# Kernel tuning notes

Hardware: AMD Instinct MI355X
Metric: run time of the kernel (lower is better)

Reference implementation:

```python
import jax, jax.numpy as jnp
import numpy as np

N_NODES = 50000
N_EDGES = 800000
C = 128
NEG_SLOPE = 0.01  # nn.LeakyReLU default


def _init_linear(key, fan_in, fan_out):
    kw, kb = jax.random.split(key)
    lim = 1.0 / np.sqrt(fan_in)
    W = jax.random.uniform(kw, (fan_in, fan_out), jnp.float32, -lim, lim)
    b = jax.random.uniform(kb, (fan_out,), jnp.float32, -lim, lim)
    return W, b


def setup_inputs() -> dict:
    key = jax.random.key(0)
    ks = jax.random.split(key, 10)
    x = jax.random.normal(ks[0], (N_NODES, C), jnp.float32)
    pos = jax.random.normal(ks[1], (N_NODES, 3), jnp.float32)
    edge_index = jax.random.randint(ks[2], (2, N_EDGES), 0, N_NODES, jnp.int64)
    # mlp_h: Linear(C,C) -> LeakyReLU -> Linear(C,3) -> Tanh
    Wh1, bh1 = _init_linear(ks[3], C, C)
    Wh2, bh2 = _init_linear(ks[4], C, 3)
    # mlp_f: Linear(C+3, C) -> LeakyReLU
    Wf, bf = _init_linear(ks[5], C + 3, C)
    # mlp_g: Linear(C,C) -> LeakyReLU -> Linear(C,C)
    Wg1, bg1 = _init_linear(ks[6], C, C)
    Wg2, bg2 = _init_linear(ks[7], C, C)
    return {"x": x, "pos": pos, "edge_index": edge_index,
            "Wh1": Wh1, "bh1": bh1, "Wh2": Wh2, "bh2": bh2,
            "Wf": Wf, "bf": bf,
            "Wg1": Wg1, "bg1": bg1, "Wg2": Wg2, "bg2": bg2}


def reference(x, pos, edge_index, Wh1, bh1, Wh2, bh2, Wf, bf, Wg1, bg1, Wg2, bg2):
    lrelu = lambda t: jax.nn.leaky_relu(t, NEG_SLOPE)
    # delta_i = tanh(mlp_h(x_i))  -> [N, 3]
    delta = jnp.tanh(lrelu(x @ Wh1 + bh1) @ Wh2 + bh2)
    src, dst = edge_index[0], edge_index[1]  # message j -> i (PyG convention)
    # per-edge relative position: pos_j - pos_i + delta_i  -> [E, 3]
    rel = pos[src] - pos[dst] + delta[dst]
    # per-edge message: mlp_f([rel, x_j])  -> [E, C]
    e = lrelu(jnp.concatenate([rel, x[src]], axis=-1) @ Wf + bf)
    # scatter-max aggregate over incoming edges per target node
    agg = jax.ops.segment_max(e, dst, num_segments=N_NODES)
    agg = jnp.where(jnp.isfinite(agg), agg, 0.0)  # empty segments -> 0
    # out_i = mlp_g(agg_i) + x_i
    out = lrelu(agg @ Wg1 + bg1) @ Wg2 + bg2 + x
    return out
```

## Files before the change

### kernel.cpp

```cpp
#include <hip/hip_runtime.h>
#include <cfloat>
#include <cmath>

#define NEG_SLOPE 0.01f

typedef __attribute__((ext_vector_type(8))) short short8;
typedef __attribute__((ext_vector_type(4))) float f32x4;

__device__ __forceinline__ float lrelu(float v) { return v >= 0.0f ? v : NEG_SLOPE * v; }

__device__ __forceinline__ ushort f2b(float f) {
    unsigned u = __float_as_uint(f);
    u += 0x7fffu + ((u >> 16) & 1u);
    return (ushort)(u >> 16);
}
__device__ __forceinline__ float b2f(ushort s) { return __uint_as_float(((unsigned)s) << 16); }

__device__ __forceinline__ void split8(const float* v, short8& hi, short8& lo) {
#pragma unroll
    for (int j = 0; j < 8; ++j) {
        ushort h = f2b(v[j]);
        hi[j] = (short)h;
        lo[j] = (short)f2b(v[j] - b2f(h));
    }
}

__global__ __launch_bounds__(256) void count_wprep_kernel(
    const int* __restrict__ ei,
    const float* __restrict__ Wh1, const float* __restrict__ Wf,
    const float* __restrict__ Wg1, const float* __restrict__ Wg2,
    ushort* __restrict__ WT, int* __restrict__ G, int E, int NBK)
{
    __shared__ int cnt[256];
    const int t = threadIdx.x;
    const int b = blockIdx.x;

    {
        int tt = b * 256 + t;
        int mat = tt >> 14;
        int idx = tt & 16383;
        int n = idx >> 7, k = idx & 127;
        float v;
        if (mat == 0)      v = Wh1[k * 128 + n];
        else if (mat == 1) v = Wf[(k + 3) * 128 + n];
        else if (mat == 2) v = Wg1[k * 128 + n];
        else               v = Wg2[k * 128 + n];
        WT[(tt - idx) + n * 128 + k] = f2b(v);
    }

    cnt[t] = 0;
    __syncthreads();
    for (int e = b * 256 + t; e < E; e += 65536)
        atomicAdd(&cnt[ei[E + e] >> 8], 1);
    __syncthreads();
    if (t < NBK) G[t * 256 + b] = cnt[t];
}

__global__ __launch_bounds__(256) void scanA_kernel(
    const int* __restrict__ G, int* __restrict__ partial)
{
    __shared__ int s[256];
    int i = blockIdx.x * 256 + threadIdx.x;
    s[threadIdx.x] = G[i];
    __syncthreads();
    for (int d = 128; d > 0; d >>= 1) {
        if (threadIdx.x < d) s[threadIdx.x] += s[threadIdx.x + d];
        __syncthreads();
    }
    if (threadIdx.x == 0) partial[blockIdx.x] = s[0];
}

__global__ __launch_bounds__(256) void scanBC_kernel(
    int* __restrict__ G, const int* __restrict__ partial, int NB)
{
    __shared__ int s[256];
    __shared__ int base;
    const int t = threadIdx.x;
    int v = (t < NB) ? partial[t] : 0;
    s[t] = v;
    __syncthreads();
    for (int d = 1; d < 256; d <<= 1) {
        int a = (t >= d) ? s[t - d] : 0;
        __syncthreads();
        s[t] += a;
        __syncthreads();
    }
    if (t == blockIdx.x) base = s[t] - v;
    __syncthreads();

    int i = blockIdx.x * 256 + t;
    int g = G[i];
    s[t] = g;
    __syncthreads();
    for (int d = 1; d < 256; d <<= 1) {
        int a = (t >= d) ? s[t - d] : 0;
        __syncthreads();
        s[t] += a;
        __syncthreads();
    }
    G[i] = base + s[t] - g;
}

__global__ __launch_bounds__(256) void partition_kernel(
    const int* __restrict__ ei, const int* __restrict__ G,
    uint* __restrict__ bpairs, int E, int NBK)
{
    __shared__ int cur[256];
    const int tid = threadIdx.x;
    if (tid < NBK) cur[tid] = G[tid * 256 + blockIdx.x];
    __syncthreads();
    for (int e = blockIdx.x * 256 + tid; e < E; e += 65536) {
        int src = ei[e];
        int dst = ei[E + e];
        int p = atomicAdd(&cur[dst >> 8], 1);
        bpairs[p] = (uint)src | ((uint)(dst & 255) << 24);
    }
}

__global__ __launch_bounds__(256) void bucket_csr_kernel(
    const uint* __restrict__ bpairs, const int* __restrict__ G,
    int* __restrict__ offs, int* __restrict__ srcs, int E, int M, int NBK)
{
    __shared__ int deg[256], scn[256], cur[256];
    const int b = blockIdx.x;
    const int t = threadIdx.x;
    const int base = G[b * 256];
    const int end  = (b + 1 < NBK) ? G[(b + 1) * 256] : E;
    deg[t] = 0;
    __syncthreads();
    for (int p = base + t; p < end; p += 256)
        atomicAdd(&deg[bpairs[p] >> 24], 1);
    __syncthreads();
    scn[t] = deg[t];
    __syncthreads();
    for (int d = 1; d < 256; d <<= 1) {
        int a = (t >= d) ? scn[t - d] : 0;
        __syncthreads();
        scn[t] += a;
        __syncthreads();
    }
    int excl = scn[t] - deg[t];
    cur[t] = excl;
    int node = b * 256 + t;
    if (node < M) offs[node] = base + excl;
    if (node == M - 1 || (b == NBK - 1 && t == 255)) offs[M] = E;
    __syncthreads();
    for (int p = base + t; p < end; p += 256) {
        uint pk = bpairs[p];
        int qpos = atomicAdd(&cur[pk >> 24], 1);
        srcs[base + qpos] = (int)(pk & 0xFFFFFFu);
    }
}


#define GEMM_CORE_REG(ACC, AH, AL)                                              \
    {                                                                           \
        _Pragma("unroll")                                                       \
        for (int ks = 0; ks < 4; ++ks) {                                        \
            _Pragma("unroll")                                                   \
            for (int nt = 0; nt < 8; ++nt) {                                    \
                short8 bfr = *(const short8*)&Bs[(nt * 16 + ln) * 136 + ks * 32 + qd * 8]; \
                ACC[nt] = __builtin_amdgcn_mfma_f32_16x16x32_bf16(AL[ks], bfr, ACC[nt], 0, 0, 0); \
                ACC[nt] = __builtin_amdgcn_mfma_f32_16x16x32_bf16(AH[ks], bfr, ACC[nt], 0, 0, 0); \
            }                                                                   \
        }                                                                       \
    }

#define STAGE_B(WTP)                                                            \
    {                                                                           \
        _Pragma("unroll")                                                       \
        for (int i = 0; i < 8; ++i) {                                           \
            int c = tid + 256 * i;                                              \
            int r = c >> 4, col8 = (c & 15) * 8;                                \
            *(uint4*)&Bs[r * 136 + col8] = *(const uint4*)((WTP) + r * 128 + col8); \
        }                                                                       \
    }

__global__ __launch_bounds__(256) void hy_kernel(
    const float* __restrict__ x, const ushort* __restrict__ Wh1T,
    const float* __restrict__ bh1, const float* __restrict__ Wh2,
    const float* __restrict__ bh2, const ushort* __restrict__ WfxT,
    const float* __restrict__ Wf, const float* __restrict__ pos,
    float* __restrict__ q, ushort* __restrict__ yb, int M)
{
    __shared__ ushort Bs[128 * 136];
    __shared__ ushort yS[64 * 128];
    const int tid = threadIdx.x;
    const int w = tid >> 6, L = tid & 63, qd = L >> 4, ln = L & 15;
    const int row0 = blockIdx.x * 64;
    const int arow = row0 + w * 16 + ln;

    short8 ah[4], al[4];
    {
        const float* base = x + (size_t)((arow < M) ? arow : 0) * 128 + qd * 8;
        float vb[8];
#pragma unroll
        for (int ks = 0; ks < 4; ++ks) {
            float4 v0 = make_float4(0.f, 0.f, 0.f, 0.f), v1 = v0;
            if (arow < M) {
                v0 = *(const float4*)(base + ks * 32);
                v1 = *(const float4*)(base + ks * 32 + 4);
            }
            vb[0] = v0.x; vb[1] = v0.y; vb[2] = v0.z; vb[3] = v0.w;
            vb[4] = v1.x; vb[5] = v1.y; vb[6] = v1.z; vb[7] = v1.w;
            split8(vb, ah[ks], al[ks]);
        }
    }

    STAGE_B(Wh1T);
    __syncthreads();
    f32x4 acc1[8];
#pragma unroll
    for (int nt = 0; nt < 8; ++nt) acc1[nt] = (f32x4){0.f, 0.f, 0.f, 0.f};
    GEMM_CORE_REG(acc1, ah, al);
    __syncthreads();

    STAGE_B(WfxT);
    __syncthreads();
    f32x4 acc2[8];
#pragma unroll
    for (int nt = 0; nt < 8; ++nt) acc2[nt] = (f32x4){0.f, 0.f, 0.f, 0.f};
    GEMM_CORE_REG(acc2, ah, al);
    __syncthreads();

    float* h1s = (float*)Bs;
#pragma unroll
    for (int nt = 0; nt < 8; ++nt) {
        int n = nt * 16 + ln;
        float bias = bh1[n];
#pragma unroll
        for (int r = 0; r < 4; ++r)
            h1s[(w * 16 + qd * 4 + r) * 132 + n] = lrelu(acc1[nt][r] + bias);
    }
#pragma unroll
    for (int r = 0; r < 4; ++r) {
        int m = w * 16 + qd * 4 + r;
        int gm = row0 + m;
        float p0 = 0.f, p1 = 0.f, p2 = 0.f;
        if (gm < M) { p0 = pos[gm * 3]; p1 = pos[gm * 3 + 1]; p2 = pos[gm * 3 + 2]; }
#pragma unroll
        for (int nt = 0; nt < 8; ++nt) {
            int n = nt * 16 + ln;
            yS[m * 128 + n] = f2b(acc2[nt][r] + p0 * Wf[n] + p1 * Wf[128 + n] + p2 * Wf[256 + n]);
        }
    }
    __syncthreads();

    int row = tid & 63, cc = tid >> 6;
    if (cc < 3 && row0 + row < M) {
        float s = 0.f;
#pragma unroll
        for (int k4 = 0; k4 < 32; ++k4) {
            float4 h = *(const float4*)&h1s[row * 132 + k4 * 4];
            s += h.x * Wh2[(k4 * 4 + 0) * 3 + cc] + h.y * Wh2[(k4 * 4 + 1) * 3 + cc]
               + h.z * Wh2[(k4 * 4 + 2) * 3 + cc] + h.w * Wh2[(k4 * 4 + 3) * 3 + cc];
        }
        q[(row0 + row) * 3 + cc] = tanhf(s + bh2[cc]) - pos[(row0 + row) * 3 + cc];
    }
#pragma unroll
    for (int i = 0; i < 4; ++i) {
        int c = tid + 256 * i;
        int r = c >> 4, col8 = (c & 15) * 8;
        if (row0 + r < M)
            *(uint4*)(yb + (size_t)(row0 + r) * 128 + col8) = *(const uint4*)&yS[r * 128 + col8];
    }
}

__global__ __launch_bounds__(256) void midout_kernel(
    const ushort* __restrict__ aggb, const float* __restrict__ qv,
    const float* __restrict__ Wf, const float* __restrict__ bfv,
    const ushort* __restrict__ Wg1T, const float* __restrict__ bg1,
    const ushort* __restrict__ Wg2T, const float* __restrict__ bg2,
    const float* __restrict__ x, float* __restrict__ out, int M)
{
    __shared__ ushort Bs[128 * 136];
    __shared__ ushort Ms[64 * 136];
    const int tid = threadIdx.x;
    const int w = tid >> 6, L = tid & 63, qd = L >> 4, ln = L & 15;
    const int row0 = blockIdx.x * 64;
    const int arow = row0 + w * 16 + ln;

    short8 ah[4], al[4];
    {
        bool ok = arow < M;
        const ushort* base = aggb + (size_t)(ok ? arow : 0) * 128 + qd * 8;
        float q0 = 0.f, q1 = 0.f, q2 = 0.f;
        if (ok) { q0 = qv[arow * 3]; q1 = qv[arow * 3 + 1]; q2 = qv[arow * 3 + 2]; }
        float vb[8];
#pragma unroll
        for (int ks = 0; ks < 4; ++ks) {
            union { uint4 u; ushort s[8]; } a;
            a.u = ok ? *(const uint4*)(base + ks * 32) : make_uint4(0xFF80FF80u, 0xFF80FF80u, 0xFF80FF80u, 0xFF80FF80u);
#pragma unroll
            for (int j = 0; j < 8; ++j) {
                int k = ks * 32 + qd * 8 + j;
                float dec = 0.f;
                if (a.s[j] != 0xFF80u)
                    dec = lrelu(b2f(a.s[j]) + q0 * Wf[k] + q1 * Wf[128 + k] + q2 * Wf[256 + k] + bfv[k]);
                vb[j] = dec;
            }
            split8(vb, ah[ks], al[ks]);
        }
    }

    STAGE_B(Wg1T);
    __syncthreads();
    f32x4 macc[8];
#pragma unroll
    for (int nt = 0; nt < 8; ++nt) macc[nt] = (f32x4){0.f, 0.f, 0.f, 0.f};
    GEMM_CORE_REG(macc, ah, al);
    __syncthreads();

#pragma unroll
    for (int nt = 0; nt < 8; ++nt) {
        int n = nt * 16 + ln;
        float bias = bg1[n];
#pragma unroll
        for (int r = 0; r < 4; ++r)
            Ms[(w * 16 + qd * 4 + r) * 136 + n] = f2b(lrelu(macc[nt][r] + bias));
    }
    STAGE_B(Wg2T);
    __syncthreads();

    short8 a2[4];
#pragma unroll
    for (int ks = 0; ks < 4; ++ks)
        a2[ks] = *(const short8*)&Ms[(w * 16 + ln) * 136 + ks * 32 + qd * 8];

    f32x4 acc2[8];
#pragma unroll
    for (int nt = 0; nt < 8; ++nt) acc2[nt] = (f32x4){0.f, 0.f, 0.f, 0.f};
#pragma unroll
    for (int ks = 0; ks < 4; ++ks) {
#pragma unroll
        for (int nt = 0; nt < 8; ++nt) {
            short8 bfr = *(const short8*)&Bs[(nt * 16 + ln) * 136 + ks * 32 + qd * 8];
            acc2[nt] = __builtin_amdgcn_mfma_f32_16x16x32_bf16(a2[ks], bfr, acc2[nt], 0, 0, 0);
        }
    }
    __syncthreads();

    float* outS = (float*)Bs;
#pragma unroll
    for (int r = 0; r < 4; ++r) {
        int m = w * 16 + qd * 4 + r;
#pragma unroll
        for (int nt = 0; nt < 8; ++nt)
            outS[m * 132 + nt * 16 + ln] = acc2[nt][r];
    }
    __syncthreads();
#pragma unroll
    for (int i = 0; i < 8; ++i) {
        int c = tid + 256 * i;
        int r = c >> 5, col4 = (c & 31) * 4;
        int gr = row0 + r;
        if (gr < M) {
            float4 o = *(const float4*)&outS[r * 132 + col4];
            float4 bv = *(const float4*)(bg2 + col4);
            float4 xv = *(const float4*)(x + (size_t)gr * 128 + col4);
            o.x += bv.x + xv.x; o.y += bv.y + xv.y;
            o.z += bv.z + xv.z; o.w += bv.w + xv.w;
            *(float4*)(out + (size_t)gr * 128 + col4) = o;
        }
    }
}

__global__ __launch_bounds__(256) void agg_kernel(
    const int* __restrict__ offs, const int* __restrict__ srcs,
    const ushort* __restrict__ yb, ushort* __restrict__ aggb, int M)
{
    int wave = threadIdx.x >> 6;
    int lane = threadIdx.x & 63;
    int node = blockIdx.x * 4 + wave;
    if (node >= M) return;
    int o0 = offs[node], o1 = offs[node + 1];
    float a0 = -INFINITY, a1 = -INFINITY;
    const uint* yp = (const uint*)yb;
    int j = o0;
    for (; j + 3 < o1; j += 4) {
        int s0 = srcs[j], s1 = srcs[j + 1], s2 = srcs[j + 2], s3 = srcs[j + 3];
        uint u0 = yp[(size_t)s0 * 64 + lane];
        uint u1 = yp[(size_t)s1 * 64 + lane];
        uint u2 = yp[(size_t)s2 * 64 + lane];
        uint u3 = yp[(size_t)s3 * 64 + lane];
        a0 = fmaxf(a0, fmaxf(fmaxf(__uint_as_float(u0 << 16), __uint_as_float(u1 << 16)),
                             fmaxf(__uint_as_float(u2 << 16), __uint_as_float(u3 << 16))));
        a1 = fmaxf(a1, fmaxf(fmaxf(__uint_as_float(u0 & 0xFFFF0000u), __uint_as_float(u1 & 0xFFFF0000u)),
                             fmaxf(__uint_as_float(u2 & 0xFFFF0000u), __uint_as_float(u3 & 0xFFFF0000u))));
    }
    for (; j < o1; ++j) {
        uint u = yp[(size_t)srcs[j] * 64 + lane];
        a0 = fmaxf(a0, __uint_as_float(u << 16));
        a1 = fmaxf(a1, __uint_as_float(u & 0xFFFF0000u));
    }
    uint pk = (__float_as_uint(a0) >> 16) | (__float_as_uint(a1) & 0xFFFF0000u);
    ((uint*)aggb)[(size_t)node * 64 + lane] = pk;
}

extern "C" void kernel_launch(void* const* d_in, const int* in_sizes, int n_in,
                              void* d_out, int out_size, void* d_ws, size_t ws_size,
                              hipStream_t stream)
{
    const float* x   = (const float*)d_in[0];
    const float* pos = (const float*)d_in[1];
    const int*   ei  = (const int*)d_in[2];
    const float* Wh1 = (const float*)d_in[3];
    const float* bh1 = (const float*)d_in[4];
    const float* Wh2 = (const float*)d_in[5];
    const float* bh2 = (const float*)d_in[6];
    const float* Wf  = (const float*)d_in[7];
    const float* bf  = (const float*)d_in[8];
    const float* Wg1 = (const float*)d_in[9];
    const float* bg1 = (const float*)d_in[10];
    const float* Wg2 = (const float*)d_in[11];
    const float* bg2 = (const float*)d_in[12];
    float* out = (float*)d_out;

    const int M = in_sizes[0] / 128;
    const int E = in_sizes[2] / 2;
    const int NBK = (M + 255) >> 8;

    char* ws = (char*)d_ws;
    size_t off = 0;
    auto alloc = [&](size_t bytes) { void* p = ws + off; off += (bytes + 255) & ~255ull; return p; };
    ushort* yb     = (ushort*)alloc((size_t)M * 128 * sizeof(ushort));
    ushort* aggb   = (ushort*)alloc((size_t)M * 128 * sizeof(ushort));
    ushort* WT     = (ushort*)alloc(4 * 16384 * sizeof(ushort));
    float*  q      = (float*)alloc((size_t)M * 3 * sizeof(float));
    int*    offs   = (int*)alloc((size_t)(M + 1) * sizeof(int));
    int*    G      = (int*)alloc((size_t)NBK * 256 * sizeof(int));
    int*    part   = (int*)alloc(256 * sizeof(int));
    uint*   bpairs = (uint*)alloc((size_t)E * sizeof(uint));
    int*    srcs   = (int*)alloc((size_t)E * sizeof(int));

    const int gb = (M + 63) / 64;

    count_wprep_kernel<<<256, 256, 0, stream>>>(ei, Wh1, Wf, Wg1, Wg2, WT, G, E, NBK);
    scanA_kernel<<<NBK, 256, 0, stream>>>(G, part);
    scanBC_kernel<<<NBK, 256, 0, stream>>>(G, part, NBK);
    partition_kernel<<<256, 256, 0, stream>>>(ei, G, bpairs, E, NBK);
    bucket_csr_kernel<<<NBK, 256, 0, stream>>>(bpairs, G, offs, srcs, E, M, NBK);

    hy_kernel<<<gb, 256, 0, stream>>>(x, WT, bh1, Wh2, bh2,
                                      WT + 16384, Wf, pos, q, yb, M);
    agg_kernel<<<(M + 3) / 4, 256, 0, stream>>>(offs, srcs, yb, aggb, M);
    midout_kernel<<<gb, 256, 0, stream>>>(aggb, q, Wf, bf,
                                          WT + 2 * 16384, bg1,
                                          WT + 3 * 16384, bg2, x, out, M);
}
```

Baseline: 219.1 us.

## Fuse scatter-max aggregation into MLP-g kernel using LDS atomicMax tiles

After: 343.5 us. 56.8% more time.

```diff
diff --git a/kernel.cpp b/kernel.cpp
--- a/kernel.cpp
+++ b/kernel.cpp
@@ -3,6 +3,7 @@
 #include <cmath>
 
 #define NEG_SLOPE 0.01f
+#define C_ELIST 2048
 
 typedef __attribute__((ext_vector_type(8))) short short8;
 typedef __attribute__((ext_vector_type(4))) float f32x4;
@@ -15,6 +16,14 @@
     return (ushort)(u >> 16);
 }
 __device__ __forceinline__ float b2f(ushort s) { return __uint_as_float(((unsigned)s) << 16); }
+
+__device__ __forceinline__ uint encb(uint b) {
+    return (b & 0x80000000u) ? ~b : (b | 0x80000000u);
+}
+__device__ __forceinline__ float decb(uint v) {
+    uint b = (v & 0x80000000u) ? (v ^ 0x80000000u) : ~v;
+    return __uint_as_float(b);
+}
 
 __device__ __forceinline__ void split8(const float* v, short8& hi, short8& lo) {
 #pragma unroll
@@ -117,41 +126,6 @@
     }
 }
 
-__global__ __launch_bounds__(256) void bucket_csr_kernel(
-    const uint* __restrict__ bpairs, const int* __restrict__ G,
-    int* __restrict__ offs, int* __restrict__ srcs, int E, int M, int NBK)
-{
-    __shared__ int deg[256], scn[256], cur[256];
-    const int b = blockIdx.x;
-    const int t = threadIdx.x;
-    const int base = G[b * 256];
-    const int end  = (b + 1 < NBK) ? G[(b + 1) * 256] : E;
-    deg[t] = 0;
-    __syncthreads();
-    for (int p = base + t; p < end; p += 256)
-        atomicAdd(&deg[bpairs[p] >> 24], 1);
-    __syncthreads();
-    scn[t] = deg[t];
-    __syncthreads();
-    for (int d = 1; d < 256; d <<= 1) {
-        int a = (t >= d) ? scn[t - d] : 0;
-        __syncthreads();
-        scn[t] += a;
-        __syncthreads();
-    }
-    int excl = scn[t] - deg[t];
-    cur[t] = excl;
-    int node = b * 256 + t;
-    if (node < M) offs[node] = base + excl;
-    if (node == M - 1 || (b == NBK - 1 && t == 255)) offs[M] = E;
-    __syncthreads();
-    for (int p = base + t; p < end; p += 256) {
-        uint pk = bpairs[p];
-        int qpos = atomicAdd(&cur[pk >> 24], 1);
-        srcs[base + qpos] = (int)(pk & 0xFFFFFFu);
-    }
-}
-
 
 #define GEMM_CORE_REG(ACC, AH, AL)                                              \
     {                                                                           \
@@ -266,42 +240,117 @@
     }
 }
 
-__global__ __launch_bounds__(256) void midout_kernel(
-    const ushort* __restrict__ aggb, const float* __restrict__ qv,
+__global__ __launch_bounds__(256) void midagg_kernel(
+    const uint* __restrict__ bpairs, const int* __restrict__ G,
+    const ushort* __restrict__ yb, const float* __restrict__ qv,
     const float* __restrict__ Wf, const float* __restrict__ bfv,
     const ushort* __restrict__ Wg1T, const float* __restrict__ bg1,
     const ushort* __restrict__ Wg2T, const float* __restrict__ bg2,
-    const float* __restrict__ x, float* __restrict__ out, int M)
+    const float* __restrict__ x, float* __restrict__ out,
+    int M, int E, int NBK)
 {
     __shared__ ushort Bs[128 * 136];
     __shared__ ushort Ms[64 * 136];
+    __shared__ int ecnt;
+    uint* tile  = (uint*)Bs;
+    uint* elist = (uint*)Ms;
     const int tid = threadIdx.x;
     const int w = tid >> 6, L = tid & 63, qd = L >> 4, ln = L & 15;
     const int row0 = blockIdx.x * 64;
-    const int arow = row0 + w * 16 + ln;
+    const int B = row0 >> 8;
+    const int lo = row0 & 255;
+    const uint* yp = (const uint*)yb;
+
+    for (int i = tid; i < 64 * 132; i += 256) tile[i] = 0u;
+    if (tid == 0) ecnt = 0;
+    __syncthreads();
+
+    const int base = G[B * 256];
+    const int end  = (B + 1 < NBK) ? G[(B + 1) * 256] : E;
+
+    for (int p = base + tid; p < end; p += 256) {
+        uint pk = bpairs[p];
+        int dl = (int)(pk >> 24) - lo;
+        if ((unsigned)dl < 64u) {
+            int idx = atomicAdd(&ecnt, 1);
+            if (idx < C_ELIST) elist[idx] = ((uint)dl << 24) | (pk & 0xFFFFFFu);
+        }
+    }
+    __syncthreads();
+    int n = ecnt;
+
+    if (n <= C_ELIST) {
+        for (int i0 = w * 8; i0 < n; i0 += 32) {
+            uint pk[8], u[8];
+#pragma unroll
+            for (int j = 0; j < 8; ++j)
+                pk[j] = (i0 + j < n) ? elist[i0 + j] : 0xFF000000u;
+#pragma unroll
+            for (int j = 0; j < 8; ++j)
+                if ((pk[j] >> 24) < 64u)
+                    u[j] = yp[(size_t)(pk[j] & 0xFFFFFFu) * 64 + L];
+#pragma unroll
+            for (int j = 0; j < 8; ++j) {
+                uint dl = pk[j] >> 24;
+                if (dl < 64u) {
+                    atomicMax(&tile[dl * 132 + 2 * L],     encb(u[j] << 16));
+                    atomicMax(&tile[dl * 132 + 2 * L + 1], encb(u[j] & 0xFFFF0000u));
+                }
+            }
+        }
+    } else {
+        for (int p0 = base + w * 8; p0 < end; p0 += 32) {
+            uint pk[8], u[8];
+#pragma unroll
+            for (int j = 0; j < 8; ++j) {
+                int p = p0 + j;
+                uint raw = (p < end) ? bpairs[p] : 0xFF000000u;
+                int dl = (int)(raw >> 24) - lo;
+                pk[j] = ((unsigned)dl < 64u) ? (((uint)dl << 24) | (raw & 0xFFFFFFu))
+                                             : 0xFF000000u;
+            }
+#pragma unroll
+            for (int j = 0; j < 8; ++j)
+                if ((pk[j] >> 24) < 64u)
+                    u[j] = yp[(size_t)(pk[j] & 0xFFFFFFu) * 64 + L];
+#pragma unroll
+            for (int j = 0; j < 8; ++j) {
+                uint dl = pk[j] >> 24;
+                if (dl < 64u) {
+                    atomicMax(&tile[dl * 132 + 2 * L],     encb(u[j] << 16));
+                    atomicMax(&tile[dl * 132 + 2 * L + 1], encb(u[j] & 0xFFFF0000u));
+                }
+            }
+        }
+    }
+    __syncthreads();
 
     short8 ah[4], al[4];
     {
-        bool ok = arow < M;
-        const ushort* base = aggb + (size_t)(ok ? arow : 0) * 128 + qd * 8;
+        const int arow_l = w * 16 + ln;
+        const int gm = row0 + arow_l;
+        bool ok = gm < M;
         float q0 = 0.f, q1 = 0.f, q2 = 0.f;
-        if (ok) { q0 = qv[arow * 3]; q1 = qv[arow * 3 + 1]; q2 = qv[arow * 3 + 2]; }
+        if (ok) { q0 = qv[gm * 3]; q1 = qv[gm * 3 + 1]; q2 = qv[gm * 3 + 2]; }
         float vb[8];
 #pragma unroll
         for (int ks = 0; ks < 4; ++ks) {
-            union { uint4 u; ushort s[8]; } a;
-            a.u = ok ? *(const uint4*)(base + ks * 32) : make_uint4(0xFF80FF80u, 0xFF80FF80u, 0xFF80FF80u, 0xFF80FF80u);
+            uint4 v0 = *(const uint4*)&tile[arow_l * 132 + ks * 32 + qd * 8];
+            uint4 v1 = *(const uint4*)&tile[arow_l * 132 + ks * 32 + qd * 8 + 4];
+            uint vv[8] = {v0.x, v0.y, v0.z, v0.w, v1.x, v1.y, v1.z, v1.w};
 #pragma unroll
             for (int j = 0; j < 8; ++j) {
                 int k = ks * 32 + qd * 8 + j;
                 float dec = 0.f;
-                if (a.s[j] != 0xFF80u)
-                    dec = lrelu(b2f(a.s[j]) + q0 * Wf[k] + q1 * Wf[128 + k] + q2 * Wf[256 + k] + bfv[k]);
+                if (ok && vv[j] != 0u)
+                    dec = lrelu(decb(vv[j]) + q0 * Wf[k] + q1 * Wf[128 + k]
+                                + q2 * Wf[256 + k] + bfv[k]);
                 vb[j] = dec;
             }
             split8(vb, ah[ks], al[ks]);
         }
     }
+    __syncthreads();
 
     STAGE_B(Wg1T);
     __syncthreads();
@@ -313,11 +362,11 @@
 
 #pragma unroll
     for (int nt = 0; nt < 8; ++nt) {
-        int n = nt * 16 + ln;
-        float bias = bg1[n];
+        int nn = nt * 16 + ln;
+        float bias = bg1[nn];
 #pragma unroll
         for (int r = 0; r < 4; ++r)
-            Ms[(w * 16 + qd * 4 + r) * 136 + n] = f2b(lrelu(macc[nt][r] + bias));
+            Ms[(w * 16 + qd * 4 + r) * 136 + nn] = f2b(lrelu(macc[nt][r] + bias));
     }
     STAGE_B(Wg2T);
     __syncthreads();
@@ -363,38 +412,6 @@
             *(float4*)(out + (size_t)gr * 128 + col4) = o;
         }
     }
-}
-
-__global__ __launch_bounds__(256) void agg_kernel(
-    const int* __restrict__ offs, const int* __restrict__ srcs,
-    const ushort* __restrict__ yb, ushort* __restrict__ aggb, int M)
-{
-    int wave = threadIdx.x >> 6;
-    int lane = threadIdx.x & 63;
-    int node = blockIdx.x * 4 + wave;
-    if (node >= M) return;
-    int o0 = offs[node], o1 = offs[node + 1];
-    float a0 = -INFINITY, a1 = -INFINITY;
-    const uint* yp = (const uint*)yb;
-    int j = o0;
-    for (; j + 3 < o1; j += 4) {
-        int s0 = srcs[j], s1 = srcs[j + 1], s2 = srcs[j + 2], s3 = srcs[j + 3];
-        uint u0 = yp[(size_t)s0 * 64 + lane];
-        uint u1 = yp[(size_t)s1 * 64 + lane];
-        uint u2 = yp[(size_t)s2 * 64 + lane];
-        uint u3 = yp[(size_t)s3 * 64 + lane];
-        a0 = fmaxf(a0, fmaxf(fmaxf(__uint_as_float(u0 << 16), __uint_as_float(u1 << 16)),
-                             fmaxf(__uint_as_float(u2 << 16), __uint_as_float(u3 << 16))));
-        a1 = fmaxf(a1, fmaxf(fmaxf(__uint_as_float(u0 & 0xFFFF0000u), __uint_as_float(u1 & 0xFFFF0000u)),
-                             fmaxf(__uint_as_float(u2 & 0xFFFF0000u), __uint_as_float(u3 & 0xFFFF0000u))));
-    }
-    for (; j < o1; ++j) {
-        uint u = yp[(size_t)srcs[j] * 64 + lane];
-        a0 = fmaxf(a0, __uint_as_float(u << 16));
-        a1 = fmaxf(a1, __uint_as_float(u & 0xFFFF0000u));
-    }
-    uint pk = (__float_as_uint(a0) >> 16) | (__float_as_uint(a1) & 0xFFFF0000u);
-    ((uint*)aggb)[(size_t)node * 64 + lane] = pk;
 }
 
 extern "C" void kernel_launch(void* const* d_in, const int* in_sizes, int n_in,
@@ -424,14 +441,11 @@
     size_t off = 0;
     auto alloc = [&](size_t bytes) { void* p = ws + off; off += (bytes + 255) & ~255ull; return p; };
     ushort* yb     = (ushort*)alloc((size_t)M * 128 * sizeof(ushort));
-    ushort* aggb   = (ushort*)alloc((size_t)M * 128 * sizeof(ushort));
     ushort* WT     = (ushort*)alloc(4 * 16384 * sizeof(ushort));
     float*  q      = (float*)alloc((size_t)M * 3 * sizeof(float));
-    int*    offs   = (int*)alloc((size_t)(M + 1) * sizeof(int));
     int*    G      = (int*)alloc((size_t)NBK * 256 * sizeof(int));
     int*    part   = (int*)alloc(256 * sizeof(int));
     uint*   bpairs = (uint*)alloc((size_t)E * sizeof(uint));
-    int*    srcs   = (int*)alloc((size_t)E * sizeof(int));
 
     const int gb = (M + 63) / 64;
 
@@ -439,12 +453,10 @@
     scanA_kernel<<<NBK, 256, 0, stream>>>(G, part);
     scanBC_kernel<<<NBK, 256, 0, stream>>>(G, part, NBK);
     partition_kernel<<<256, 256, 0, stream>>>(ei, G, bpairs, E, NBK);
-    bucket_csr_kernel<<<NBK, 256, 0, stream>>>(bpairs, G, offs, srcs, E, M, NBK);
 
     hy_kernel<<<gb, 256, 0, stream>>>(x, WT, bh1, Wh2, bh2,
                                       WT + 16384, Wf, pos, q, yb, M);
-    agg_kernel<<<(M + 3) / 4, 256, 0, stream>>>(offs, srcs, yb, aggb, M);
-    midout_kernel<<<gb, 256, 0, stream>>>(aggb, q, Wf, bf,
+    midagg_kernel<<<gb, 256, 0, stream>>>(bpairs, G, yb, q, Wf, bf,
                                           WT + 2 * 16384, bg1,
-                                          WT + 3 * 16384, bg2, x, out, M);
-}
+                                          WT + 3 * 16384, bg2, x, out, M, E, NBK);
+}
```
